# Kernel tuning notes

Measured on AMD Instinct MI355X. Metric: run time of the kernel, lower is better.

The kernel has to match this reference:

```python
import jax, jax.numpy as jnp
import numpy as np

BS, NC, Nc, D_n = 8, 256, 128, 64
ALPHA, HS, HM = 2, 256, 128
GAMMA_MAX = 0.5
EPS = 1e-6


def setup_inputs() -> dict:
    key = jax.random.key(0)
    ks = jax.random.split(key, 12)
    f = jax.random.normal
    return {
        "x": f(ks[0], (BS, NC, D_n), jnp.float32),
        "h": f(ks[1], (BS, NC, Nc, D_n), jnp.float32) * 0.1,
        "W": f(ks[2], (BS, NC, Nc, Nc), jnp.float32) * (Nc ** -0.5),
        "decay": jax.random.uniform(ks[3], (BS, NC, Nc), jnp.float32),
        "hebbian": f(ks[4], (BS, NC, Nc, Nc), jnp.float32) * 0.01,
        "neuron_id": f(ks[5], (NC, Nc, D_n), jnp.float32) * (D_n ** -0.5),
        "state_w1": f(ks[6], (HS, 2 * D_n), jnp.float32) * ((2 * D_n) ** -0.5),
        "state_b1": jnp.zeros((HS,), jnp.float32),
        "state_w2": f(ks[7], (D_n, HS), jnp.float32) * (HS ** -0.5),
        "state_b2": jnp.zeros((D_n,), jnp.float32),
        "msg_w1": f(ks[8], (HM, D_n), jnp.float32) * (D_n ** -0.5),
        "msg_b1": jnp.zeros((HM,), jnp.float32),
        "msg_w2": f(ks[9], (D_n, HM), jnp.float32) * (HM ** -0.5),
        "msg_b2": jnp.zeros((D_n,), jnp.float32),
        "inject_w": f(ks[10], (NC, ALPHA * D_n, D_n), jnp.float32) * (D_n ** -0.5),
        "inject_b": jnp.zeros((NC, ALPHA * D_n), jnp.float32),
        "W_decay_logit": jnp.full((NC, Nc), -3.0, jnp.float32),
        "decay_gamma_logit": jnp.full((NC, Nc), -3.0, jnp.float32),
        "hebbian_decay_logit": jnp.full((NC, Nc), 2.0, jnp.float32),
    }


def _rms_norm(v):
    # F.rms_norm over the last (Nc) axis, no affine weight
    return v * jax.lax.rsqrt(jnp.mean(v * v, axis=-1, keepdims=True) + EPS)


def reference(x, h, W, decay, hebbian, neuron_id,
              state_w1, state_b1, state_w2, state_b2,
              msg_w1, msg_b1, msg_w2, msg_b2,
              inject_w, inject_b,
              W_decay_logit, decay_gamma_logit, hebbian_decay_logit):
    B = x.shape[0]
    # per-cell injection of external input into the first ALPHA neurons
    inj = jnp.einsum('bcd,cad->bca', x, inject_w) + inject_b   # [B,NC,ALPHA*D_n]
    h = h.at[:, :, :ALPHA, :].add(inj.reshape(B, NC, ALPHA, D_n))
    h_id = h + neuron_id                                       # identity embedding broadcast
    # per-neuron message MLP (tanh hidden)
    m = jnp.tanh(jnp.einsum('bcnd,hd->bcnh', h_id, msg_w1) + msg_b1)
    m = jnp.einsum('bcnh,dh->bcnd', m, msg_w2) + msg_b2        # [B,NC,Nc,D_n]
    # Hebbian-weighted adjacency message passing: small per-cell matmul W @ m
    agg = jnp.einsum('bcij,bcjd->bcid', W, m)
    # state update MLP on concat(state, aggregated message)
    s = jnp.tanh(jnp.einsum('bcnd,hd->bcnh',
                            jnp.concatenate([h_id, agg], axis=-1), state_w1) + state_b1)
    dh = jnp.einsum('bcnh,dh->bcnd', s, state_w2) + state_b2
    # gated decay of per-neuron state
    dg = GAMMA_MAX * jax.nn.sigmoid(decay_gamma_logit)         # [NC,Nc]
    decay_new = (1.0 - dg) * decay + dg * jax.nn.sigmoid(jnp.mean(dh, axis=-1))
    h_new = (1.0 - decay_new[..., None]) * h + decay_new[..., None] * jnp.tanh(dh)
    # Hebbian outer-product plasticity
    hg = GAMMA_MAX * jax.nn.sigmoid(hebbian_decay_logit)
    outer = jnp.einsum('bcid,bcjd->bcij', h_new, m) / D_n
    hebbian_new = (1.0 - hg[..., None]) * hebbian + hg[..., None] * outer
    # decayed adjacency update + rms-norm over the incoming-edge axis
    wg = GAMMA_MAX * jax.nn.sigmoid(W_decay_logit)
    W_new = _rms_norm((1.0 - wg[..., None]) * W + wg[..., None] * hebbian_new)
    return (h_new, m, W_new, decay_new, hebbian_new)
```

## Files before the change

kernel.cpp:

```cpp
#include <hip/hip_runtime.h>


#define NCELL 256

typedef __attribute__((ext_vector_type(8))) short bf16x8;
typedef __attribute__((ext_vector_type(4))) float f32x4;

#define MFMA(a, b, c) __builtin_amdgcn_mfma_f32_16x16x32_bf16((a), (b), (c), 0, 0, 0)

__device__ __forceinline__ unsigned short f2bf(float f) {
    unsigned u = __builtin_bit_cast(unsigned, f);
    u = (u + 0x7FFFu + ((u >> 16) & 1u)) >> 16;
    return (unsigned short)u;
}
__device__ __forceinline__ float bf2f(unsigned short b) {
    unsigned u = ((unsigned)b) << 16;
    return __builtin_bit_cast(float, u);
}
__device__ __forceinline__ float frcp(float x) { return __builtin_amdgcn_rcpf(x); }
__device__ __forceinline__ float sigm(float v) { return frcp(1.0f + __expf(-v)); }
__device__ __forceinline__ float ftanh(float x) {
    float e = __expf(2.0f * x);
    return 1.0f - 2.0f * frcp(e + 1.0f);
}

__device__ __forceinline__ int sw64(int row, int col) {
    return row * 64 + ((((col >> 3) ^ row) & 7) << 3) + (col & 7);
}
__device__ __forceinline__ int sw128(int row, int col) {
    return row * 128 + (((col >> 3) ^ (row & 7)) << 3) + (col & 7);
}
__device__ __forceinline__ int sw32(int row, int col) {
    return row * 32 + ((((col >> 3) ^ row) & 3) << 3) + (col & 7);
}

__global__ void cvt_w(const float* __restrict__ a, const float* __restrict__ b,
                      const float* __restrict__ c, const float* __restrict__ d,
                      unsigned short* __restrict__ dst) {
    int i = blockIdx.x * 256 + threadIdx.x;
    float v;
    if (i < 8192) v = a[i];
    else if (i < 16384) v = b[i - 8192];
    else if (i < 49152) v = c[i - 16384];
    else v = d[i - 49152];
    dst[i] = f2bf(v);
}

__global__ __launch_bounds__(256, 3)
void cell_kernel(const float* __restrict__ x, const float* __restrict__ h,
                 const float* __restrict__ W, const float* __restrict__ decay,
                 const float* __restrict__ hebb, const float* __restrict__ nid,
                 const float* __restrict__ sb1, const float* __restrict__ sb2,
                 const float* __restrict__ mb1, const float* __restrict__ mb2,
                 const float* __restrict__ injw, const float* __restrict__ injb,
                 const float* __restrict__ wdl, const float* __restrict__ dgl,
                 const float* __restrict__ hdl,
                 const unsigned short* __restrict__ wbf,
                 float* __restrict__ out) {
    const int cell = blockIdx.x;
    const int c = cell & (NCELL - 1);
    const int tid = threadIdx.x;
    const int wv = tid >> 6;
    const int lane = tid & 63;
    const int lr = lane & 15;
    const int lg = lane >> 4;

    float* out_h  = out;
    float* out_m  = out + 16777216;
    float* out_W  = out + 33554432;
    float* out_d  = out + 67108864;
    float* out_hb = out + 67371008;

    const unsigned short* w1m = wbf;
    const unsigned short* w2m = wbf + 8192;
    const unsigned short* w1s = wbf + 16384;
    const unsigned short* w2s = wbf + 49152;

    __shared__ alignas(16) unsigned char smem[49664];
    unsigned short* m_s  = (unsigned short*)smem;
    unsigned short* mT_s = (unsigned short*)(smem + 16384);
    unsigned short* st_s = (unsigned short*)(smem + 32768);
    float* inj_s = (float*)(smem + 49152);
    unsigned short* hbuf = st_s + wv * 2048;

    float4 wpa[4][2][2];
    {
        const float* Wbase = W + (size_t)cell * 16384;
        #pragma unroll
        for (int ks = 0; ks < 4; ++ks)
            #pragma unroll
            for (int rt = 0; rt < 2; ++rt) {
                const float* wr = Wbase + (wv * 32 + rt * 16 + lr) * 128 + ks * 32 + lg * 8;
                wpa[ks][rt][0] = *(const float4*)wr;
                wpa[ks][rt][1] = *(const float4*)(wr + 4);
            }
    }

    if (tid < 128) {
        const float* iwr = injw + (c * 128 + tid) * 64;
        const float* xr = x + cell * 64;
        float acc = injb[c * 128 + tid];
        #pragma unroll
        for (int d4 = 0; d4 < 16; ++d4) {
            float4 a = ((const float4*)iwr)[d4];
            float4 xv = ((const float4*)xr)[d4];
            acc += a.x * xv.x + a.y * xv.y + a.z * xv.z + a.w * xv.w;
        }
        inj_s[tid] = acc;
    }
    __syncthreads();

    bf16x8 aH[2][2];
    #pragma unroll
    for (int rt = 0; rt < 2; ++rt)
        #pragma unroll
        for (int ks = 0; ks < 2; ++ks) {
            const int row = wv * 32 + rt * 16 + lr;
            const int col = ks * 32 + lg * 8;
            const float* hr = h + (size_t)(cell * 128 + row) * 64 + col;
            const float* nr = nid + (size_t)(c * 128 + row) * 64 + col;
            float4 a0 = *(const float4*)hr;
            float4 a1 = *(const float4*)(hr + 4);
            float4 n0 = *(const float4*)nr;
            float4 n1 = *(const float4*)(nr + 4);
            float v[8] = {a0.x, a0.y, a0.z, a0.w, a1.x, a1.y, a1.z, a1.w};
            float nn[8] = {n0.x, n0.y, n0.z, n0.w, n1.x, n1.y, n1.z, n1.w};
            unsigned short us[8];
            #pragma unroll
            for (int j = 0; j < 8; ++j) {
                float hv = v[j] + nn[j];
                if (row < 2) hv += inj_s[row * 64 + col + j];
                us[j] = f2bf(hv);
            }
            aH[rt][ks] = *(bf16x8*)us;
        }

    f32x4 accM[2][4];
    #pragma unroll
    for (int rt = 0; rt < 2; ++rt)
        #pragma unroll
        for (int dt = 0; dt < 4; ++dt)
            accM[rt][dt] = (f32x4){0.f, 0.f, 0.f, 0.f};

    #pragma unroll
    for (int ch = 0; ch < 4; ++ch) {
        f32x4 accH[2][2];
        #pragma unroll
        for (int rt = 0; rt < 2; ++rt)
            #pragma unroll
            for (int ht = 0; ht < 2; ++ht)
                accH[rt][ht] = (f32x4){0.f, 0.f, 0.f, 0.f};
        #pragma unroll
        for (int ks = 0; ks < 2; ++ks)
            #pragma unroll
            for (int ht = 0; ht < 2; ++ht) {
                bf16x8 bw = *(const bf16x8*)&w1m[(ch * 32 + ht * 16 + lr) * 64 + ks * 32 + lg * 8];
                #pragma unroll
                for (int rt = 0; rt < 2; ++rt)
                    accH[rt][ht] = MFMA(aH[rt][ks], bw, accH[rt][ht]);
            }
        #pragma unroll
        for (int rt = 0; rt < 2; ++rt)
            #pragma unroll
            for (int ht = 0; ht < 2; ++ht) {
                float b1v = mb1[ch * 32 + ht * 16 + lr];
                #pragma unroll
                for (int r = 0; r < 4; ++r) {
                    float t = ftanh(accH[rt][ht][r] + b1v);
                    hbuf[sw32(rt * 16 + lg * 4 + r, ht * 16 + lr)] = f2bf(t);
                }
            }
        #pragma unroll
        for (int rt = 0; rt < 2; ++rt) {
            bf16x8 aM = *(const bf16x8*)&hbuf[sw32(rt * 16 + lr, lg * 8)];
            #pragma unroll
            for (int dt = 0; dt < 4; ++dt) {
                bf16x8 bw = *(const bf16x8*)&w2m[(dt * 16 + lr) * 128 + ch * 32 + lg * 8];
                accM[rt][dt] = MFMA(aM, bw, accM[rt][dt]);
            }
        }
    }
    #pragma unroll
    for (int rt = 0; rt < 2; ++rt)
        #pragma unroll
        for (int dt = 0; dt < 4; ++dt) {
            float b2v = mb2[dt * 16 + lr];
            #pragma unroll
            for (int r = 0; r < 4; ++r) {
                float mv = accM[rt][dt][r] + b2v;
                int n = wv * 32 + rt * 16 + lg * 4 + r;
                int dcol = dt * 16 + lr;
                out_m[(size_t)(cell * 128 + n) * 64 + dcol] = mv;
                unsigned short mb = f2bf(mv);
                m_s[sw64(n, dcol)] = mb;
                mT_s[sw128(dcol, n)] = mb;
            }
        }
    __syncthreads();

    f32x4 accA[2][4];
    #pragma unroll
    for (int rt = 0; rt < 2; ++rt)
        #pragma unroll
        for (int dt = 0; dt < 4; ++dt)
            accA[rt][dt] = (f32x4){0.f, 0.f, 0.f, 0.f};
    #pragma unroll
    for (int ks = 0; ks < 4; ++ks)
        #pragma unroll
        for (int rt = 0; rt < 2; ++rt) {
            float4 wa = wpa[ks][rt][0];
            float4 wb = wpa[ks][rt][1];
            unsigned short uw[8] = {f2bf(wa.x), f2bf(wa.y), f2bf(wa.z), f2bf(wa.w),
                                    f2bf(wb.x), f2bf(wb.y), f2bf(wb.z), f2bf(wb.w)};
            bf16x8 aW = *(bf16x8*)uw;
            #pragma unroll
            for (int dt = 0; dt < 4; ++dt) {
                bf16x8 bm = *(const bf16x8*)&mT_s[sw128(dt * 16 + lr, ks * 32 + lg * 8)];
                accA[rt][dt] = MFMA(aW, bm, accA[rt][dt]);
            }
        }
    #pragma unroll
    for (int rt = 0; rt < 2; ++rt)
        #pragma unroll
        for (int dt = 0; dt < 4; ++dt)
            #pragma unroll
            for (int r = 0; r < 4; ++r)
                st_s[sw64(wv * 32 + rt * 16 + lg * 4 + r, dt * 16 + lr)] = f2bf(accA[rt][dt][r]);

    bf16x8 aG[2][2];
    #pragma unroll
    for (int rt = 0; rt < 2; ++rt)
        #pragma unroll
        for (int ks = 0; ks < 2; ++ks)
            aG[rt][ks] = *(const bf16x8*)&st_s[sw64(wv * 32 + rt * 16 + lr, ks * 32 + lg * 8)];

    f32x4 accD[2][4];
    #pragma unroll
    for (int rt = 0; rt < 2; ++rt)
        #pragma unroll
        for (int dt = 0; dt < 4; ++dt)
            accD[rt][dt] = (f32x4){0.f, 0.f, 0.f, 0.f};

    #pragma unroll
    for (int ch = 0; ch < 8; ++ch) {
        f32x4 accS[2][2];
        #pragma unroll
        for (int rt = 0; rt < 2; ++rt)
            #pragma unroll
            for (int ht = 0; ht < 2; ++ht)
                accS[rt][ht] = (f32x4){0.f, 0.f, 0.f, 0.f};
        #pragma unroll
        for (int ks = 0; ks < 4; ++ks)
            #pragma unroll
            for (int ht = 0; ht < 2; ++ht) {
                bf16x8 bw = *(const bf16x8*)&w1s[(ch * 32 + ht * 16 + lr) * 128 + ks * 32 + lg * 8];
                #pragma unroll
                for (int rt = 0; rt < 2; ++rt) {
                    bf16x8 af = (ks < 2) ? aH[rt][ks] : aG[rt][ks - 2];
                    accS[rt][ht] = MFMA(af, bw, accS[rt][ht]);
                }
            }
        #pragma unroll
        for (int rt = 0; rt < 2; ++rt)
            #pragma unroll
            for (int ht = 0; ht < 2; ++ht) {
                float bv = sb1[ch * 32 + ht * 16 + lr];
                #pragma unroll
                for (int r = 0; r < 4; ++r) {
                    float t = ftanh(accS[rt][ht][r] + bv);
                    hbuf[sw32(rt * 16 + lg * 4 + r, ht * 16 + lr)] = f2bf(t);
                }
            }
        #pragma unroll
        for (int rt = 0; rt < 2; ++rt) {
            bf16x8 aS = *(const bf16x8*)&hbuf[sw32(rt * 16 + lr, lg * 8)];
            #pragma unroll
            for (int dt = 0; dt < 4; ++dt) {
                bf16x8 bw = *(const bf16x8*)&w2s[(dt * 16 + lr) * 256 + ch * 32 + lg * 8];
                accD[rt][dt] = MFMA(aS, bw, accD[rt][dt]);
            }
        }
    }

    float dnew_r[2][4];
    #pragma unroll
    for (int rt = 0; rt < 2; ++rt)
        #pragma unroll
        for (int r = 0; r < 4; ++r) {
            float s = 0.f;
            #pragma unroll
            for (int dt = 0; dt < 4; ++dt) {
                accD[rt][dt][r] += sb2[dt * 16 + lr];
                s += accD[rt][dt][r];
            }
            s += __shfl_xor(s, 1);
            s += __shfl_xor(s, 2);
            s += __shfl_xor(s, 4);
            s += __shfl_xor(s, 8);
            int row = wv * 32 + rt * 16 + lg * 4 + r;
            float mean = s * (1.0f / 64.0f);
            float dg = 0.5f * sigm(dgl[c * 128 + row]);
            float dn = (1.0f - dg) * decay[cell * 128 + row] + dg * sigm(mean);
            if (lr == 0) out_d[cell * 128 + row] = dn;
            dnew_r[rt][r] = dn;
        }
    #pragma unroll
    for (int rt = 0; rt < 2; ++rt)
        #pragma unroll
        for (int r = 0; r < 4; ++r) {
            int row = wv * 32 + rt * 16 + lg * 4 + r;
            float dn = dnew_r[rt][r];
            const float* hr = h + (size_t)(cell * 128 + row) * 64;
            #pragma unroll
            for (int dt = 0; dt < 4; ++dt) {
                int col = dt * 16 + lr;
                float hpost = hr[col];
                if (row < 2) hpost += inj_s[row * 64 + col];
                float hn = (1.0f - dn) * hpost + dn * ftanh(accD[rt][dt][r]);
                out_h[(size_t)(cell * 128 + row) * 64 + col] = hn;
                st_s[sw64(row, col)] = f2bf(hn);
            }
        }

    bf16x8 aO[2][2];
    #pragma unroll
    for (int rt = 0; rt < 2; ++rt)
        #pragma unroll
        for (int ks = 0; ks < 2; ++ks)
            aO[rt][ks] = *(const bf16x8*)&st_s[sw64(wv * 32 + rt * 16 + lr, ks * 32 + lg * 8)];

    f32x4 accO[2][8];
    #pragma unroll
    for (int rt = 0; rt < 2; ++rt)
        #pragma unroll
        for (int jt = 0; jt < 8; ++jt)
            accO[rt][jt] = (f32x4){0.f, 0.f, 0.f, 0.f};
    #pragma unroll
    for (int jt = 0; jt < 8; ++jt)
        #pragma unroll
        for (int ks = 0; ks < 2; ++ks) {
            bf16x8 bm = *(const bf16x8*)&m_s[sw64(jt * 16 + lr, ks * 32 + lg * 8)];
            #pragma unroll
            for (int rt = 0; rt < 2; ++rt)
                accO[rt][jt] = MFMA(aO[rt][ks], bm, accO[rt][jt]);
        }

    #pragma unroll
    for (int rt = 0; rt < 2; ++rt)
        #pragma unroll
        for (int r = 0; r < 4; ++r) {
            int i = wv * 32 + rt * 16 + lg * 4 + r;
            float hg = 0.5f * sigm(hdl[c * 128 + i]);
            float wg = 0.5f * sigm(wdl[c * 128 + i]);
            const float* hbr = hebb + (size_t)(cell * 128 + i) * 128;
            const float* Wr = W + (size_t)(cell * 128 + i) * 128;
            float* ohb = out_hb + (size_t)(cell * 128 + i) * 128;
            float wpre[8];
            float ss = 0.f;
            #pragma unroll
            for (int jt = 0; jt < 8; ++jt) {
                int j = jt * 16 + lr;
                float o = accO[rt][jt][r] * (1.0f / 64.0f);
                float hbn = (1.0f - hg) * hbr[j] + hg * o;
                ohb[j] = hbn;
                float wp = (1.0f - wg) * Wr[j] + wg * hbn;
                wpre[jt] = wp;
                ss += wp * wp;
            }
            ss += __shfl_xor(ss, 1);
            ss += __shfl_xor(ss, 2);
            ss += __shfl_xor(ss, 4);
            ss += __shfl_xor(ss, 8);
            float scale = rsqrtf(ss * (1.0f / 128.0f) + 1e-6f);
            float* oW = out_W + (size_t)(cell * 128 + i) * 128;
            #pragma unroll
            for (int jt = 0; jt < 8; ++jt)
                oW[jt * 16 + lr] = wpre[jt] * scale;
        }
}

extern "C" void kernel_launch(void* const* d_in, const int* in_sizes, int n_in,
                              void* d_out, int out_size, void* d_ws, size_t ws_size,
                              hipStream_t stream) {
    const float* x    = (const float*)d_in[0];
    const float* h    = (const float*)d_in[1];
    const float* W    = (const float*)d_in[2];
    const float* dec  = (const float*)d_in[3];
    const float* hebb = (const float*)d_in[4];
    const float* nid  = (const float*)d_in[5];
    const float* sw1  = (const float*)d_in[6];
    const float* sb1  = (const float*)d_in[7];
    const float* sw2  = (const float*)d_in[8];
    const float* sb2  = (const float*)d_in[9];
    const float* mw1  = (const float*)d_in[10];
    const float* mb1  = (const float*)d_in[11];
    const float* mw2  = (const float*)d_in[12];
    const float* mb2  = (const float*)d_in[13];
    const float* injw = (const float*)d_in[14];
    const float* injb = (const float*)d_in[15];
    const float* wdl  = (const float*)d_in[16];
    const float* dgl  = (const float*)d_in[17];
    const float* hdl  = (const float*)d_in[18];

    unsigned short* wbf = (unsigned short*)d_ws;

    cvt_w<<<256, 256, 0, stream>>>(mw1, mw2, sw1, sw2, wbf);
    cell_kernel<<<2048, 256, 0, stream>>>(x, h, W, dec, hebb, nid, sb1, sb2, mb1, mb2,
                                          injw, injb, wdl, dgl, hdl, wbf, (float*)d_out);
}
```

Baseline: 355.1 us.

## Split Hebbian/W update into separate kernel to cut LDS and registers

Moves the Hebbian outer-product and W rms-norm update into a second kernel that re-reads h_new and m from the output buffer and converts them to bf16 in shared memory. The main cell kernel drops the m_s buffer and the h_new staging, which reduces LDS to about 33KB, and its launch bound is raised to allow 4 blocks per SM. The injection matvec now runs on one wave with two outputs per lane, and the barrier right after it is removed. The trade-off is an extra launch plus a global round trip for h_new and m, about 64MB more traffic, and the removed sync relies on later barriers to order inj_s.

```diff
diff --git a/kernel.cpp b/kernel.cpp
--- a/kernel.cpp
+++ b/kernel.cpp
@@ -5,6 +5,7 @@
 
 typedef __attribute__((ext_vector_type(8))) short bf16x8;
 typedef __attribute__((ext_vector_type(4))) float f32x4;
+typedef __attribute__((ext_vector_type(4))) unsigned short u16x4;
 
 #define MFMA(a, b, c) __builtin_amdgcn_mfma_f32_16x16x32_bf16((a), (b), (c), 0, 0, 0)
 
@@ -12,10 +13,6 @@
     unsigned u = __builtin_bit_cast(unsigned, f);
     u = (u + 0x7FFFu + ((u >> 16) & 1u)) >> 16;
     return (unsigned short)u;
-}
-__device__ __forceinline__ float bf2f(unsigned short b) {
-    unsigned u = ((unsigned)b) << 16;
-    return __builtin_bit_cast(float, u);
 }
 __device__ __forceinline__ float frcp(float x) { return __builtin_amdgcn_rcpf(x); }
 __device__ __forceinline__ float sigm(float v) { return frcp(1.0f + __expf(-v)); }
@@ -46,15 +43,14 @@
     dst[i] = f2bf(v);
 }
 
-__global__ __launch_bounds__(256, 3)
+__global__ __launch_bounds__(256, 4)
 void cell_kernel(const float* __restrict__ x, const float* __restrict__ h,
                  const float* __restrict__ W, const float* __restrict__ decay,
-                 const float* __restrict__ hebb, const float* __restrict__ nid,
+                 const float* __restrict__ nid,
                  const float* __restrict__ sb1, const float* __restrict__ sb2,
                  const float* __restrict__ mb1, const float* __restrict__ mb2,
                  const float* __restrict__ injw, const float* __restrict__ injb,
-                 const float* __restrict__ wdl, const float* __restrict__ dgl,
-                 const float* __restrict__ hdl,
+                 const float* __restrict__ dgl,
                  const unsigned short* __restrict__ wbf,
                  float* __restrict__ out) {
     const int cell = blockIdx.x;
@@ -65,22 +61,19 @@
     const int lr = lane & 15;
     const int lg = lane >> 4;
 
-    float* out_h  = out;
-    float* out_m  = out + 16777216;
-    float* out_W  = out + 33554432;
-    float* out_d  = out + 67108864;
-    float* out_hb = out + 67371008;
+    float* out_h = out;
+    float* out_m = out + 16777216;
+    float* out_d = out + 67108864;
 
     const unsigned short* w1m = wbf;
     const unsigned short* w2m = wbf + 8192;
     const unsigned short* w1s = wbf + 16384;
     const unsigned short* w2s = wbf + 49152;
 
-    __shared__ alignas(16) unsigned char smem[49664];
-    unsigned short* m_s  = (unsigned short*)smem;
-    unsigned short* mT_s = (unsigned short*)(smem + 16384);
-    unsigned short* st_s = (unsigned short*)(smem + 32768);
-    float* inj_s = (float*)(smem + 49152);
+    __shared__ alignas(16) unsigned char smem[33280];
+    unsigned short* mT_s = (unsigned short*)smem;
+    unsigned short* st_s = (unsigned short*)(smem + 16384);
+    float* inj_s = (float*)(smem + 32768);
     unsigned short* hbuf = st_s + wv * 2048;
 
     float4 wpa[4][2][2];
@@ -96,19 +89,23 @@
             }
     }
 
-    if (tid < 128) {
-        const float* iwr = injw + (c * 128 + tid) * 64;
+    if (wv == 0) {
         const float* xr = x + cell * 64;
-        float acc = injb[c * 128 + tid];
+        const float* i0 = injw + (c * 128 + lane) * 64;
+        const float* i1 = i0 + 64 * 64;
+        float acc0 = injb[c * 128 + lane];
+        float acc1 = injb[c * 128 + 64 + lane];
         #pragma unroll
         for (int d4 = 0; d4 < 16; ++d4) {
-            float4 a = ((const float4*)iwr)[d4];
             float4 xv = ((const float4*)xr)[d4];
-            acc += a.x * xv.x + a.y * xv.y + a.z * xv.z + a.w * xv.w;
-        }
-        inj_s[tid] = acc;
+            float4 a = ((const float4*)i0)[d4];
+            float4 b = ((const float4*)i1)[d4];
+            acc0 += a.x * xv.x + a.y * xv.y + a.z * xv.z + a.w * xv.w;
+            acc1 += b.x * xv.x + b.y * xv.y + b.z * xv.z + b.w * xv.w;
+        }
+        inj_s[lane] = acc0;
+        inj_s[64 + lane] = acc1;
     }
-    __syncthreads();
 
     bf16x8 aH[2][2];
     #pragma unroll
@@ -191,9 +188,7 @@
                 int n = wv * 32 + rt * 16 + lg * 4 + r;
                 int dcol = dt * 16 + lr;
                 out_m[(size_t)(cell * 128 + n) * 64 + dcol] = mv;
-                unsigned short mb = f2bf(mv);
-                m_s[sw64(n, dcol)] = mb;
-                mT_s[sw128(dcol, n)] = mb;
+                mT_s[sw128(dcol, n)] = f2bf(mv);
             }
         }
     __syncthreads();
@@ -318,16 +313,50 @@
                 if (row < 2) hpost += inj_s[row * 64 + col];
                 float hn = (1.0f - dn) * hpost + dn * ftanh(accD[rt][dt][r]);
                 out_h[(size_t)(cell * 128 + row) * 64 + col] = hn;
-                st_s[sw64(row, col)] = f2bf(hn);
-            }
-        }
+            }
+        }
+}
+
+__global__ __launch_bounds__(256, 4)
+void hebb_kernel(const float* __restrict__ W, const float* __restrict__ hebb,
+                 const float* __restrict__ wdl, const float* __restrict__ hdl,
+                 float* __restrict__ out) {
+    const int cell = blockIdx.x;
+    const int c = cell & (NCELL - 1);
+    const int tid = threadIdx.x;
+    const int wv = tid >> 6;
+    const int lane = tid & 63;
+    const int lr = lane & 15;
+    const int lg = lane >> 4;
+
+    const float* hsrc = out + (size_t)cell * 8192;
+    const float* msrc = out + 16777216 + (size_t)cell * 8192;
+    float* out_W  = out + 33554432;
+    float* out_hb = out + 67371008;
+
+    __shared__ alignas(16) unsigned char smem[32768];
+    unsigned short* hA = (unsigned short*)smem;
+    unsigned short* mB = (unsigned short*)(smem + 16384);
+
+    #pragma unroll
+    for (int g = 0; g < 8; ++g) {
+        int idx = g * 1024 + tid * 4;
+        int row = idx >> 6, col = idx & 63;
+        float4 hv = *(const float4*)(hsrc + idx);
+        float4 mv = *(const float4*)(msrc + idx);
+        u16x4 hu = {f2bf(hv.x), f2bf(hv.y), f2bf(hv.z), f2bf(hv.w)};
+        u16x4 mu = {f2bf(mv.x), f2bf(mv.y), f2bf(mv.z), f2bf(mv.w)};
+        *(u16x4*)&hA[sw64(row, col)] = hu;
+        *(u16x4*)&mB[sw64(row, col)] = mu;
+    }
+    __syncthreads();
 
     bf16x8 aO[2][2];
     #pragma unroll
     for (int rt = 0; rt < 2; ++rt)
         #pragma unroll
         for (int ks = 0; ks < 2; ++ks)
-            aO[rt][ks] = *(const bf16x8*)&st_s[sw64(wv * 32 + rt * 16 + lr, ks * 32 + lg * 8)];
+            aO[rt][ks] = *(const bf16x8*)&hA[sw64(wv * 32 + rt * 16 + lr, ks * 32 + lg * 8)];
 
     f32x4 accO[2][8];
     #pragma unroll
@@ -339,7 +368,7 @@
     for (int jt = 0; jt < 8; ++jt)
         #pragma unroll
         for (int ks = 0; ks < 2; ++ks) {
-            bf16x8 bm = *(const bf16x8*)&m_s[sw64(jt * 16 + lr, ks * 32 + lg * 8)];
+            bf16x8 bm = *(const bf16x8*)&mB[sw64(jt * 16 + lr, ks * 32 + lg * 8)];
             #pragma unroll
             for (int rt = 0; rt < 2; ++rt)
                 accO[rt][jt] = MFMA(aO[rt][ks], bm, accO[rt][jt]);
@@ -405,6 +434,7 @@
     unsigned short* wbf = (unsigned short*)d_ws;
 
     cvt_w<<<256, 256, 0, stream>>>(mw1, mw2, sw1, sw2, wbf);
-    cell_kernel<<<2048, 256, 0, stream>>>(x, h, W, dec, hebb, nid, sb1, sb2, mb1, mb2,
-                                          injw, injb, wdl, dgl, hdl, wbf, (float*)d_out);
-}
+    cell_kernel<<<2048, 256, 0, stream>>>(x, h, W, dec, nid, sb1, sb2, mb1, mb2,
+                                          injw, injb, dgl, wbf, (float*)d_out);
+    hebb_kernel<<<2048, 256, 0, stream>>>(W, hebb, wdl, hdl, (float*)d_out);
+}
```

Result: slower. 376.0 us (+5.9%).
